# Optimization experiments

Measured on AMD Instinct MI355X. Metric: run time of the kernel, lower is better.

Reference implementation:

```python
import jax, jax.numpy as jnp
import numpy as np

B, P, S, D, L = 8, 64, 512, 512, 64


def setup_inputs() -> dict:
    key = jax.random.key(0)
    ks = jax.random.split(key, 12)
    span_repr = jax.random.normal(ks[0], (B, S, D), dtype=jnp.float32)
    predicates = jax.random.randint(ks[1], (B, P), 0, S, dtype=jnp.int64)
    labels = jax.random.randint(ks[2], (B, P, S), 0, L, dtype=jnp.int64)
    long_mask = jnp.ones((B, P, S), dtype=jnp.int64)
    sc = 1.0 / np.sqrt(D)
    # last-layer weights of FFNN linear_p / linear_a (only last layer matters in source)
    Wp = jax.random.normal(ks[3], (D, D), dtype=jnp.float32) * sc
    bp = jnp.zeros((D,), dtype=jnp.float32)
    Wa = jax.random.normal(ks[4], (D, D), dtype=jnp.float32) * sc
    ba = jnp.zeros((D,), dtype=jnp.float32)
    wp = jax.random.normal(ks[5], (D,), dtype=jnp.float32) * sc  # W_p (Linear D->1, no bias)
    wa = jax.random.normal(ks[6], (D,), dtype=jnp.float32) * sc  # W_a
    W1 = jax.random.normal(ks[7], (L, D, D), dtype=jnp.float32) * sc
    W2 = jax.random.normal(ks[8], (2 * D, L), dtype=jnp.float32) * sc
    b = jax.random.normal(ks[9], (1, L), dtype=jnp.float32) * 0.02
    return {"span_repr": span_repr, "predicates": predicates, "labels": labels,
            "long_mask": long_mask, "Wp": Wp, "bp": bp, "Wa": Wa, "ba": ba,
            "wp": wp, "wa": wa, "W1": W1, "W2": W2, "b": b}


def reference(span_repr, predicates, labels, long_mask, Wp, bp, Wa, ba, wp, wa, W1, W2, b):
    d = span_repr.shape[-1]
    # gather predicate representations: [B, P, D]
    pred_repr = jnp.take_along_axis(span_repr, predicates[..., None], axis=1)
    # FFNN (only last layer is effective in source) + scalar projections
    predicates_score = jax.nn.relu(pred_repr @ Wp.T + bp) @ wp        # [B, P]
    argument_score = jax.nn.relu(span_repr @ Wa.T + ba) @ wa          # [B, S]
    p_a_score = predicates_score[:, :, None] + argument_score[:, None, :]  # [B, P, S]
    # biaffine term: matmul(matmul(pred, W1), span^T) -> [B, P, S, L]
    first = jnp.einsum('bpd,lde,bse->bpsl', pred_repr, W1, span_repr)
    # concat(pred, span) @ W2, split to avoid materializing the concat
    second = (jnp.einsum('bpd,dl->bpl', pred_repr, W2[:d])[:, :, None, :]
              + jnp.einsum('bsd,dl->bsl', span_repr, W2[d:])[:, None, :, :])
    combine = first + second + b + p_a_score[..., None]               # [B, P, S, L]
    combine = combine.at[..., -1].set(0.0)
    num_labels = combine.shape[-1]
    # long_mask is all ones, so masked_select is the full flatten
    stack_instance = combine.reshape(-1, num_labels)                  # [B*P*S, L]
    stack_label = labels.reshape(-1)                                  # [B*P*S]
    return stack_instance, stack_label
```

## Files before the change

### kernel.cpp

```cpp
#include <hip/hip_runtime.h>
#include <hip/hip_bf16.h>

typedef __bf16 bf16x8 __attribute__((ext_vector_type(8)));
typedef float f32x4 __attribute__((ext_vector_type(4)));
typedef unsigned short ushort_t;

#define SS 512
#define DD 512
#define LL 64

__device__ __forceinline__ ushort_t f2b(float f) {
    union { float f; unsigned u; } x; x.f = f;
    unsigned r = x.u + 0x7FFFu + ((x.u >> 16) & 1u);
    return (ushort_t)(r >> 16);
}

__device__ __forceinline__ void async16(const void* g, void* l) {
    __builtin_amdgcn_global_load_lds(
        (const __attribute__((address_space(1))) unsigned int*)g,
        (__attribute__((address_space(3))) unsigned int*)l, 16, 0, 0);
}

__device__ __forceinline__ void stage_tile(const ushort_t* __restrict__ A, int lda,
                                           const ushort_t* __restrict__ Bt, int ldb,
                                           int k0, ushort_t* buf) {
    const int t = threadIdx.x;
    const int wbase = (t >> 6) << 10;
#pragma unroll
    for (int p = 0; p < 2; p++) {
        int row = (p << 7) + (t >> 2);
        int kg = (t & 3) ^ ((t >> 3) & 3);
        async16(A + (size_t)row * lda + k0 + kg * 8,
                (char*)buf + (p << 13) + wbase);
        async16(Bt + (size_t)row * ldb + k0 + kg * 8,
                (char*)(buf + 8192) + (p << 13) + wbase);
    }
}

__device__ __forceinline__ void gemm256(const ushort_t* __restrict__ A, int lda,
                                        const ushort_t* __restrict__ Bt, int ldb,
                                        ushort_t* lds, f32x4 (&acc)[8][4]) {
    const int t = threadIdx.x;
    const int lane = t & 63, wid = t >> 6;
    const int wm = wid >> 2, wn = wid & 3;
    const int r15 = lane & 15, kg = lane >> 4;
    const int sx = ((kg ^ ((r15 >> 1) & 3)) << 4);
    const f32x4 z4 = {0.f, 0.f, 0.f, 0.f};
#pragma unroll
    for (int i = 0; i < 8; i++)
#pragma unroll
        for (int j = 0; j < 4; j++) acc[i][j] = z4;

    stage_tile(A, lda, Bt, ldb, 0, lds);
    stage_tile(A, lda, Bt, ldb, 32, lds + 16384);

    for (int T = 0; T < 16; ++T) {
        if (T < 15) asm volatile("s_waitcnt vmcnt(4)" ::: "memory");
        else        asm volatile("s_waitcnt vmcnt(0)" ::: "memory");
        __builtin_amdgcn_s_barrier();
        __builtin_amdgcn_sched_barrier(0);
        const ushort_t* bufA = lds + (T % 3) * 16384;
        const ushort_t* bufB = bufA + 8192;
        const char* pa = (const char*)bufA + (wm * 128 + r15) * 64 + sx;
        const char* pb = (const char*)bufB + (wn * 64 + r15) * 64 + sx;
        bf16x8 af[8], bf[4];
#pragma unroll
        for (int mf = 0; mf < 8; mf++) af[mf] = *(const bf16x8*)(pa + mf * 1024);
#pragma unroll
        for (int nf = 0; nf < 4; nf++) bf[nf] = *(const bf16x8*)(pb + nf * 1024);
        if (T + 2 < 16)
            stage_tile(A, lda, Bt, ldb, (T + 2) * 32, lds + ((T + 2) % 3) * 16384);
#pragma unroll
        for (int mf = 0; mf < 8; mf++)
#pragma unroll
            for (int nf = 0; nf < 4; nf++)
                acc[mf][nf] = __builtin_amdgcn_mfma_f32_16x16x32_bf16(
                    af[mf], bf[nf], acc[mf][nf], 0, 0, 0);
    }
    __syncthreads();
}

__device__ __forceinline__ void stageA(const ushort_t* __restrict__ A,
                                       int k0, ushort_t* buf) {
    const int t = threadIdx.x;
    const int wbase = (t >> 6) << 10;
#pragma unroll
    for (int p = 0; p < 2; p++) {
        int row = (p << 7) + (t >> 2);
        int kg = (t & 3) ^ ((t >> 3) & 3);
        async16(A + (size_t)row * DD + k0 + kg * 8, (char*)buf + (p << 13) + wbase);
    }
}

__device__ __forceinline__ void gemm256_w1(const ushort_t* __restrict__ predB,
                                           const float* __restrict__ W1le,
                                           ushort_t* lds, f32x4 (&acc)[8][4]) {
    const int t = threadIdx.x;
    const int lane = t & 63, wid = t >> 6;
    const int wm = wid >> 2, wn = wid & 3;
    const int r15 = lane & 15, kg = lane >> 4;
    const int sx = ((kg ^ ((r15 >> 1) & 3)) << 4);
    const f32x4 z4 = {0.f, 0.f, 0.f, 0.f};
#pragma unroll
    for (int i = 0; i < 8; i++)
#pragma unroll
        for (int j = 0; j < 4; j++) acc[i][j] = z4;

    const float* bbase = W1le + (size_t)(kg * 8) * DD + wn * 64 + r15;
    float fb[4][8];
    auto loadB = [&](int k0) {
#pragma unroll
        for (int nf = 0; nf < 4; nf++)
#pragma unroll
            for (int j = 0; j < 8; j++)
                fb[nf][j] = bbase[(size_t)(k0 + j) * DD + nf * 16];
    };

    stageA(predB, 0, lds);
    loadB(0);
    stageA(predB, 32, lds + 8192);

    for (int T = 0; T < 16; ++T) {
        if (T < 15) asm volatile("s_waitcnt vmcnt(2)" ::: "memory");
        else        asm volatile("s_waitcnt vmcnt(0)" ::: "memory");
        __builtin_amdgcn_s_barrier();
        __builtin_amdgcn_sched_barrier(0);
        bf16x8 bf[4];
#pragma unroll
        for (int nf = 0; nf < 4; nf++)
#pragma unroll
            for (int j = 0; j < 8; j++) bf[nf][j] = (__bf16)fb[nf][j];
        if (T + 1 < 16) loadB((T + 1) * 32);
        if (T + 2 < 16) stageA(predB, (T + 2) * 32, lds + ((T + 2) % 3) * 8192);
        const char* pa = (const char*)(lds + (T % 3) * 8192)
                         + (wm * 128 + r15) * 64 + sx;
        bf16x8 af[8];
#pragma unroll
        for (int mf = 0; mf < 8; mf++) af[mf] = *(const bf16x8*)(pa + mf * 1024);
#pragma unroll
        for (int mf = 0; mf < 8; mf++)
#pragma unroll
            for (int nf = 0; nf < 4; nf++)
                acc[mf][nf] = __builtin_amdgcn_mfma_f32_16x16x32_bf16(
                    af[mf], bf[nf], acc[mf][nf], 0, 0, 0);
    }
    __syncthreads();
}

__global__ void __launch_bounds__(512, 2) k_U_small(
    const ushort_t* __restrict__ predB, const float* __restrict__ W1,
    ushort_t* __restrict__ UB,
    const ushort_t* __restrict__ spanB, const ushort_t* __restrict__ WaB,
    const ushort_t* __restrict__ WpB, const ushort_t* __restrict__ W2bT,
    const ushort_t* __restrict__ W2aT,
    const float* __restrict__ ba_, const float* __restrict__ bp_,
    const float* __restrict__ wa, const float* __restrict__ wp,
    float* ascore, float* pscore, float* spanW2, float* predW2) {
    extern __shared__ ushort_t lds[];
    const f32x4 z4 = {0.f, 0.f, 0.f, 0.f};
    const int t = threadIdx.x, lane = t & 63;
    const int r15 = lane & 15, kg = lane >> 4;
    if (blockIdx.x < 256) {
        f32x4 acc[8][4];
        int swz = (blockIdx.x & 7) * 32 + (blockIdx.x >> 3);
        int m0 = (swz & 1) * 256, n0 = (swz >> 1) * 256;
        int l = n0 >> 9, e0 = n0 & 511;
        gemm256_w1(predB + (size_t)m0 * DD, W1 + ((size_t)l * DD) * DD + e0, lds, acc);
        const int wid = t >> 6;
        const int wm = wid >> 2, wn = wid & 3;
        ushort_t* my = lds + wid * 4096;
        int gm = m0 + wm * 128, gn = n0 + wn * 64;
#pragma unroll
        for (int ch = 0; ch < 2; ch++) {
#pragma unroll
            for (int mf2 = 0; mf2 < 4; mf2++)
#pragma unroll
                for (int nf = 0; nf < 4; nf++)
#pragma unroll
                    for (int j = 0; j < 4; j++)
                        my[(mf2 * 16 + kg * 4 + j) * 64 + nf * 16 + r15] =
                            f2b(acc[ch * 4 + mf2][nf][j]);
#pragma unroll
            for (int it = 0; it < 8; it++) {
                int lr = it * 8 + (lane >> 3);
                bf16x8 v = *(const bf16x8*)(my + lr * 64 + (lane & 7) * 8);
                *(bf16x8*)(UB + (size_t)(gm + ch * 64 + lr) * 32768 + gn
                           + (lane & 7) * 8) = v;
            }
        }
        return;
    }
    const bool act = t < 256;
    ushort_t* As = lds;
    ushort_t* Bs = lds + 4096;
    const int wid4 = (t >> 6) & 3;
    const int o0 = wid4 * 1024 + lane * 16;
    int blk = blockIdx.x - 256;
    if (blk < 144) {
        const ushort_t *A, *Bt; const float *bias, *w; float* sc; int m0, n0;
        if (blk < 128) { A = spanB; Bt = WaB; bias = ba_; w = wa; sc = ascore;
                         m0 = (blk >> 2) * 128; n0 = (blk & 3) * 128; }
        else { int q = blk - 128; A = predB; Bt = WpB; bias = bp_; w = wp; sc = pscore;
               m0 = (q >> 2) * 128; n0 = (q & 3) * 128; }
        const ushort_t* Ab = A + (size_t)m0 * DD;
        const ushort_t* Bb = Bt + (size_t)n0 * DD;
        f32x4 acc[4][4];
#pragma unroll
        for (int i = 0; i < 4; i++)
#pragma unroll
            for (int j = 0; j < 4; j++) acc[i][j] = z4;
        int wr = (wid4 >> 1) * 64, wc = (wid4 & 1) * 64;
        for (int k0 = 0; k0 < DD; k0 += 32) {
            if (act) {
#pragma unroll
                for (int p = 0; p < 2; p++) {
                    int o = o0 + p * 4096;
                    async16(Ab + (size_t)(o >> 6) * DD + k0 + ((o & 63) >> 1), (char*)As + o);
                    async16(Bb + (size_t)(o >> 6) * DD + k0 + ((o & 63) >> 1), (char*)Bs + o);
                }
            }
            __syncthreads();
            if (act) {
                bf16x8 af[4], bf[4];
#pragma unroll
                for (int mf = 0; mf < 4; mf++)
                    af[mf] = *(const bf16x8*)(As + (wr + mf * 16 + r15) * 32 + kg * 8);
#pragma unroll
                for (int nf = 0; nf < 4; nf++)
                    bf[nf] = *(const bf16x8*)(Bs + (wc + nf * 16 + r15) * 32 + kg * 8);
#pragma unroll
                for (int mf = 0; mf < 4; mf++)
#pragma unroll
                    for (int nf = 0; nf < 4; nf++)
                        acc[mf][nf] = __builtin_amdgcn_mfma_f32_16x16x32_bf16(
                            af[mf], bf[nf], acc[mf][nf], 0, 0, 0);
            }
            __syncthreads();
        }
        if (act) {
#pragma unroll
            for (int mf = 0; mf < 4; mf++)
#pragma unroll
                for (int j = 0; j < 4; j++) {
                    float v = 0.f;
#pragma unroll
                    for (int nf = 0; nf < 4; nf++) {
                        int col = n0 + wc + nf * 16 + r15;
                        float c = acc[mf][nf][j] + bias[col];
                        if (c > 0.f) v += c * w[col];
                    }
                    v += __shfl_xor(v, 1); v += __shfl_xor(v, 2);
                    v += __shfl_xor(v, 4); v += __shfl_xor(v, 8);
                    if (r15 == 0) atomicAdd(&sc[m0 + wr + mf * 16 + kg * 4 + j], v);
                }
        }
    } else {
        int q = blk - 144;
        const ushort_t *A, *Bt; float* C; int m0;
        if (q < 32) { A = spanB; Bt = W2bT; C = spanW2; m0 = q * 128; }
        else { A = predB; Bt = W2aT; C = predW2; m0 = (q - 32) * 128; }
        const ushort_t* Ab = A + (size_t)m0 * DD;
        f32x4 acc[4][2];
#pragma unroll
        for (int i = 0; i < 4; i++) { acc[i][0] = z4; acc[i][1] = z4; }
        int wr = (wid4 >> 1) * 64, wc = (wid4 & 1) * 32;
        for (int k0 = 0; k0 < DD; k0 += 32) {
            if (act) {
#pragma unroll
                for (int p = 0; p < 2; p++) {
                    int o = o0 + p * 4096;
                    async16(Ab + (size_t)(o >> 6) * DD + k0 + ((o & 63) >> 1), (char*)As + o);
                }
                int o = o0;
                async16(Bt + (size_t)(o >> 6) * DD + k0 + ((o & 63) >> 1), (char*)Bs + o);
            }
            __syncthreads();
            if (act) {
                bf16x8 af[4], bf[2];
#pragma unroll
                for (int mf = 0; mf < 4; mf++)
                    af[mf] = *(const bf16x8*)(As + (wr + mf * 16 + r15) * 32 + kg * 8);
#pragma unroll
                for (int nf = 0; nf < 2; nf++)
                    bf[nf] = *(const bf16x8*)(Bs + (wc + nf * 16 + r15) * 32 + kg * 8);
#pragma unroll
                for (int mf = 0; mf < 4; mf++)
#pragma unroll
                    for (int nf = 0; nf < 2; nf++)
                        acc[mf][nf] = __builtin_amdgcn_mfma_f32_16x16x32_bf16(
                            af[mf], bf[nf], acc[mf][nf], 0, 0, 0);
            }
            __syncthreads();
        }
        if (act) {
#pragma unroll
            for (int mf = 0; mf < 4; mf++)
#pragma unroll
                for (int nf = 0; nf < 2; nf++)
#pragma unroll
                    for (int j = 0; j < 4; j++) {
                        int m = m0 + wr + mf * 16 + kg * 4 + j;
                        int n = wc + nf * 16 + r15;
                        C[(size_t)m * LL + n] = acc[mf][nf][j];
                    }
        }
    }
}

__global__ void __launch_bounds__(512, 2) k_out256(const ushort_t* __restrict__ spanB,
    const ushort_t* __restrict__ UB, const float* __restrict__ spanW2,
    const float* __restrict__ predW2, const float* __restrict__ ascore,
    const float* __restrict__ pscore, const float* __restrict__ bias,
    float* __restrict__ out) {
    extern __shared__ ushort_t lds[];
    f32x4 acc[8][4];
    int swz = (blockIdx.x & 7) * 32 + (blockIdx.x >> 3);
    int b = swz >> 5, r = swz & 31;
    int m0 = (r & 1) * 256, n0 = (r >> 1) * 256;
    gemm256(spanB + ((size_t)b * SS + m0) * DD, DD,
            UB + ((size_t)b * 4096 + n0) * DD, DD, lds, acc);
    const int t = threadIdx.x, lane = t & 63, wid = t >> 6;
    const int wm = wid >> 2, wn = wid & 3, r15 = lane & 15, kg = lane >> 4;
    float cn[4]; int nn[4];
#pragma unroll
    for (int nf = 0; nf < 4; nf++) {
        int n = n0 + wn * 64 + nf * 16 + r15;
        nn[nf] = n;
        cn[nf] = bias[n & 63] + predW2[b * 4096 + n] + pscore[b * 64 + (n >> 6)];
    }
#pragma unroll
    for (int mf = 0; mf < 8; mf++)
#pragma unroll
        for (int j = 0; j < 4; j++) {
            int s = m0 + wm * 128 + mf * 16 + kg * 4 + j;
            float as_ = ascore[b * SS + s];
            const float* sw = spanW2 + ((size_t)b * SS + s) * LL;
#pragma unroll
            for (int nf = 0; nf < 4; nf++) {
                int n = nn[nf], l = n & 63, p = n >> 6;
                float v = acc[mf][nf][j] + cn[nf] + as_ + sw[l];
                if (l == LL - 1) v = 0.f;
                out[(((size_t)b * 64 + p) * SS + s) * LL + l] = v;
            }
        }
}

__global__ __launch_bounds__(256) void k_prep(
    const float* __restrict__ span, const int* __restrict__ preds,
    const int* __restrict__ labels, const float* __restrict__ Wa,
    const float* __restrict__ Wp, const float* __restrict__ W2,
    ushort_t* spanB, ushort_t* predB, ushort_t* WaB, ushort_t* WpB,
    ushort_t* W2aT, ushort_t* W2bT, float* out, float* scores) {
    int blk = blockIdx.x;
    if (blk < 4096) {
        int id = blk * 256 + threadIdx.x;
        if (id < 524288) {
            float4 v = ((const float4*)span)[id];
            ((ushort4*)spanB)[id] = make_ushort4(f2b(v.x), f2b(v.y), f2b(v.z), f2b(v.w));
        } else if (id < 589824) {
            int j = id - 524288;
            int row = j >> 7, c4 = j & 127;
            int b = row >> 6;
            int idx = preds[row];
            float4 v = ((const float4*)(span + ((size_t)(b * SS + idx)) * DD))[c4];
            ((ushort4*)(predB + (size_t)row * DD))[c4] =
                make_ushort4(f2b(v.x), f2b(v.y), f2b(v.z), f2b(v.w));
        } else if (id < 851968) {
            int k = id - 589824;
            out[16777216 + k] = (float)labels[k];
        } else if (id < 917504) {
            int j = id - 851968;
            float4 v = ((const float4*)Wa)[j];
            ((ushort4*)WaB)[j] = make_ushort4(f2b(v.x), f2b(v.y), f2b(v.z), f2b(v.w));
        } else if (id < 983040) {
            int j = id - 917504;
            float4 v = ((const float4*)Wp)[j];
            ((ushort4*)WpB)[j] = make_ushort4(f2b(v.x), f2b(v.y), f2b(v.z), f2b(v.w));
        } else if (id < 1015808) {
            int j = id - 983040;
            W2aT[j] = f2b(W2[(size_t)(j & 511) * LL + (j >> 9)]);
        } else {
            int j = id - 1015808;
            W2bT[j] = f2b(W2[(size_t)((j & 511) + DD) * LL + (j >> 9)]);
        }
    } else {
        int idx = (blk - 4096) * 256 + threadIdx.x;
        if (idx < 4608) scores[idx] = 0.f;
    }
}

extern "C" void kernel_launch(void* const* d_in, const int* in_sizes, int n_in,
                              void* d_out, int out_size, void* d_ws, size_t ws_size,
                              hipStream_t stream) {
    const float* span   = (const float*)d_in[0];
    const int*   preds  = (const int*)d_in[1];
    const int*   labels = (const int*)d_in[2];
    const float* Wp     = (const float*)d_in[4];
    const float* bp_    = (const float*)d_in[5];
    const float* Wa     = (const float*)d_in[6];
    const float* ba_    = (const float*)d_in[7];
    const float* wp     = (const float*)d_in[8];
    const float* wa     = (const float*)d_in[9];
    const float* W1     = (const float*)d_in[10];
    const float* W2     = (const float*)d_in[11];
    const float* bias   = (const float*)d_in[12];
    float* out = (float*)d_out;
    char* ws = (char*)d_ws;

    ushort_t* spanB  = (ushort_t*)(ws + 0);
    ushort_t* predB  = (ushort_t*)(ws + 4194304);
    ushort_t* WaB    = (ushort_t*)(ws + 4718592);
    ushort_t* WpB    = (ushort_t*)(ws + 5242880);
    ushort_t* W2aT   = (ushort_t*)(ws + 5767168);
    ushort_t* W2bT   = (ushort_t*)(ws + 5832704);
    ushort_t* UB     = (ushort_t*)(ws + 39452672);
    float*    ascore = (float*)(ws + 73007104);
    float*    pscore = (float*)(ws + 73023488);
    float*    spanW2 = (float*)(ws + 73025536);
    float*    predW2 = (float*)(ws + 74074112);

    hipFuncSetAttribute((const void*)k_U_small,
                        hipFuncAttributeMaxDynamicSharedMemorySize, 65536);
    hipFuncSetAttribute((const void*)k_out256,
                        hipFuncAttributeMaxDynamicSharedMemorySize, 98304);

    k_prep<<<4114, 256, 0, stream>>>(span, preds, labels, Wa, Wp, W2,
                                     spanB, predB, WaB, WpB, W2aT, W2bT,
                                     out, ascore);

    k_U_small<<<436, 512, 65536, stream>>>(predB, W1, UB,
                                           spanB, WaB, WpB, W2bT, W2aT,
                                           ba_, bp_, wa, wp,
                                           ascore, pscore, spanW2, predW2);

    k_out256<<<256, 512, 98304, stream>>>(spanB, UB, spanW2, predW2,
                                          ascore, pscore, bias, out);
}
```

Measured before the change: 84.25 us.

## Stage W1 tiles through LDS with coalesced float2 loads and double buffering

In the U GEMM, the old code read fp32 W1 straight into registers with strided scalar loads. It now reads W1 with coalesced float2 loads along the row, converts to bf16, and writes a transposed, padded tile (72-byte row pitch) into LDS. The B operand is then read from LDS as MFMA fragments. The A/B pipeline becomes a two-stage double buffer with full vmcnt(0) waits and two barriers per iteration, where before it was a three-stage async pipeline. LDS use grows to 69632 bytes, and the block-to-tile swizzle is changed as well. The aim is to cut uncoalesced global traffic on the large W1 read. The cost is extra LDS writes, more synchronisation, and less prefetch depth.

```diff
diff --git a/kernel.cpp b/kernel.cpp
--- a/kernel.cpp
+++ b/kernel.cpp
@@ -80,8 +80,8 @@
     __syncthreads();
 }
 
-__device__ __forceinline__ void stageA(const ushort_t* __restrict__ A,
-                                       int k0, ushort_t* buf) {
+__device__ __forceinline__ void stageA2(const ushort_t* __restrict__ A,
+                                        int k0, ushort_t* buf) {
     const int t = threadIdx.x;
     const int wbase = (t >> 6) << 10;
 #pragma unroll
@@ -92,9 +92,9 @@
     }
 }
 
-__device__ __forceinline__ void gemm256_w1(const ushort_t* __restrict__ predB,
-                                           const float* __restrict__ W1le,
-                                           ushort_t* lds, f32x4 (&acc)[8][4]) {
+__device__ __forceinline__ void gemm256_w1t(const ushort_t* __restrict__ predB,
+                                            const float* __restrict__ W1g,
+                                            ushort_t* lds, f32x4 (&acc)[8][4]) {
     const int t = threadIdx.x;
     const int lane = t & 63, wid = t >> 6;
     const int wm = wid >> 2, wn = wid & 3;
@@ -106,45 +106,70 @@
 #pragma unroll
         for (int j = 0; j < 4; j++) acc[i][j] = z4;
 
-    const float* bbase = W1le + (size_t)(kg * 8) * DD + wn * 64 + r15;
-    float fb[4][8];
+    const int kpair = t >> 5;
+    const int e2 = (t & 31) * 2;
+    const float* r0base = W1g + (size_t)(2 * kpair) * DD + e2;
+    float2 v0[4], v1[4];
     auto loadB = [&](int k0) {
-#pragma unroll
-        for (int nf = 0; nf < 4; nf++)
-#pragma unroll
-            for (int j = 0; j < 8; j++)
-                fb[nf][j] = bbase[(size_t)(k0 + j) * DD + nf * 16];
+        const float* p0 = r0base + (size_t)k0 * DD;
+        const float* p1 = p0 + DD;
+#pragma unroll
+        for (int i = 0; i < 4; i++) {
+            v0[i] = *(const float2*)(p0 + 64 * i);
+            v1[i] = *(const float2*)(p1 + 64 * i);
+        }
     };
-
-    stageA(predB, 0, lds);
+    auto writeB = [&](ushort_t* bbuf) {
+        char* base = (char*)bbuf;
+#pragma unroll
+        for (int i = 0; i < 4; i++) {
+            int e = e2 + 64 * i;
+            unsigned w0 = (unsigned)f2b(v0[i].x) | ((unsigned)f2b(v1[i].x) << 16);
+            unsigned w1 = (unsigned)f2b(v0[i].y) | ((unsigned)f2b(v1[i].y) << 16);
+            *(unsigned*)(base + (size_t)e * 72 + kpair * 4) = w0;
+            *(unsigned*)(base + (size_t)(e + 1) * 72 + kpair * 4) = w1;
+        }
+    };
+    ushort_t* A0 = lds;            ushort_t* A1 = lds + 8192;
+    ushort_t* B0 = lds + 16384;    ushort_t* B1 = lds + 25600;
+
     loadB(0);
-    stageA(predB, 32, lds + 8192);
+    stageA2(predB, 0, A0);
+    asm volatile("s_waitcnt vmcnt(0)" ::: "memory");
+    writeB(B0);
+    __syncthreads();
 
     for (int T = 0; T < 16; ++T) {
-        if (T < 15) asm volatile("s_waitcnt vmcnt(2)" ::: "memory");
-        else        asm volatile("s_waitcnt vmcnt(0)" ::: "memory");
-        __builtin_amdgcn_s_barrier();
-        __builtin_amdgcn_sched_barrier(0);
+        ushort_t* Acur = (T & 1) ? A1 : A0;
+        ushort_t* Bcur = (T & 1) ? B1 : B0;
+        ushort_t* Anxt = (T & 1) ? A0 : A1;
+        ushort_t* Bnxt = (T & 1) ? B0 : B1;
+        if (T + 1 < 16) { loadB((T + 1) * 32); stageA2(predB, (T + 1) * 32, Anxt); }
+        const char* pa = (const char*)Acur + (wm * 128 + r15) * 64 + sx;
+        bf16x8 af[8];
+#pragma unroll
+        for (int mf = 0; mf < 8; mf++) af[mf] = *(const bf16x8*)(pa + mf * 1024);
         bf16x8 bf[4];
-#pragma unroll
-        for (int nf = 0; nf < 4; nf++)
-#pragma unroll
-            for (int j = 0; j < 8; j++) bf[nf][j] = (__bf16)fb[nf][j];
-        if (T + 1 < 16) loadB((T + 1) * 32);
-        if (T + 2 < 16) stageA(predB, (T + 2) * 32, lds + ((T + 2) % 3) * 8192);
-        const char* pa = (const char*)(lds + (T % 3) * 8192)
-                         + (wm * 128 + r15) * 64 + sx;
-        bf16x8 af[8];
-#pragma unroll
-        for (int mf = 0; mf < 8; mf++) af[mf] = *(const bf16x8*)(pa + mf * 1024);
+        const char* pb = (const char*)Bcur + (size_t)(wn * 64 + r15) * 72 + kg * 16;
+#pragma unroll
+        for (int nf = 0; nf < 4; nf++) {
+            union { bf16x8 v; uint2 q[2]; } u;
+            const char* pn = pb + (size_t)nf * 16 * 72;
+            u.q[0] = *(const uint2*)(pn);
+            u.q[1] = *(const uint2*)(pn + 8);
+            bf[nf] = u.v;
+        }
 #pragma unroll
         for (int mf = 0; mf < 8; mf++)
 #pragma unroll
             for (int nf = 0; nf < 4; nf++)
                 acc[mf][nf] = __builtin_amdgcn_mfma_f32_16x16x32_bf16(
                     af[mf], bf[nf], acc[mf][nf], 0, 0, 0);
-    }
-    __syncthreads();
+        asm volatile("s_waitcnt vmcnt(0)" ::: "memory");
+        __syncthreads();
+        if (T + 1 < 16) writeB(Bnxt);
+        __syncthreads();
+    }
 }
 
 __global__ void __launch_bounds__(512, 2) k_U_small(
@@ -162,10 +187,12 @@
     const int r15 = lane & 15, kg = lane >> 4;
     if (blockIdx.x < 256) {
         f32x4 acc[8][4];
-        int swz = (blockIdx.x & 7) * 32 + (blockIdx.x >> 3);
-        int m0 = (swz & 1) * 256, n0 = (swz >> 1) * 256;
-        int l = n0 >> 9, e0 = n0 & 511;
-        gemm256_w1(predB + (size_t)m0 * DD, W1 + ((size_t)l * DD) * DD + e0, lds, acc);
+        int x = blockIdx.x & 7, s = blockIdx.x >> 3;
+        int m0 = (s & 1) * 256;
+        int nidx = x * 16 + (s >> 1);
+        int n0 = nidx * 256, l = nidx >> 1, e0 = (nidx & 1) * 256;
+        gemm256_w1t(predB + (size_t)m0 * DD,
+                    W1 + (size_t)l * DD * DD + e0, lds, acc);
         const int wid = t >> 6;
         const int wm = wid >> 2, wn = wid & 3;
         ushort_t* my = lds + wid * 4096;
@@ -420,7 +447,7 @@
     float*    predW2 = (float*)(ws + 74074112);
 
     hipFuncSetAttribute((const void*)k_U_small,
-                        hipFuncAttributeMaxDynamicSharedMemorySize, 65536);
+                        hipFuncAttributeMaxDynamicSharedMemorySize, 69632);
     hipFuncSetAttribute((const void*)k_out256,
                         hipFuncAttributeMaxDynamicSharedMemorySize, 98304);
 
@@ -428,7 +455,7 @@
                                      spanB, predB, WaB, WpB, W2aT, W2bT,
                                      out, ascore);
 
-    k_U_small<<<436, 512, 65536, stream>>>(predB, W1, UB,
+    k_U_small<<<436, 512, 69632, stream>>>(predB, W1, UB,
                                            spanB, WaB, WpB, W2bT, W2aT,
                                            ba_, bp_, wa, wp,
                                            ascore, pscore, spanW2, predW2);
```

After: 94.99 us. 1.13x slower.

## Shrink W1 GEMM tiles to 128x128 with 256-thread blocks in k_U_small

Applied to the files above, without the earlier changes.

The U = pred·W1 GEMM in k_U_small moves from 256x256 tiles on 512-thread blocks to 128x128 tiles on 256-thread blocks, giving 1024 tiles instead of 256. The small score and W2 GEMM blocks are now placed first in the grid, and their idle half of threads is removed so every thread participates. The aim is better load balance and occupancy across CUs, with less LDS per block. The cost is that each fp32 W1 element is reloaded by four M-tiles instead of two, and the smaller tiles do fewer MFMAs per byte loaded.

```diff
diff --git a/kernel.cpp b/kernel.cpp
--- a/kernel.cpp
+++ b/kernel.cpp
@@ -80,33 +80,33 @@
     __syncthreads();
 }
 
-__device__ __forceinline__ void stageA(const ushort_t* __restrict__ A,
-                                       int k0, ushort_t* buf) {
+__device__ __forceinline__ void stageA128(const ushort_t* __restrict__ A,
+                                          int k0, ushort_t* buf) {
     const int t = threadIdx.x;
-    const int wbase = (t >> 6) << 10;
 #pragma unroll
     for (int p = 0; p < 2; p++) {
-        int row = (p << 7) + (t >> 2);
+        int row = (p << 6) + (t >> 2);
         int kg = (t & 3) ^ ((t >> 3) & 3);
-        async16(A + (size_t)row * DD + k0 + kg * 8, (char*)buf + (p << 13) + wbase);
-    }
-}
-
-__device__ __forceinline__ void gemm256_w1(const ushort_t* __restrict__ predB,
-                                           const float* __restrict__ W1le,
-                                           ushort_t* lds, f32x4 (&acc)[8][4]) {
+        async16(A + (size_t)row * DD + k0 + kg * 8,
+                (char*)buf + (p << 12) + ((t >> 6) << 10) + (t & 63) * 16);
+    }
+}
+
+__device__ __forceinline__ void gemm128_w1(const ushort_t* __restrict__ predB,
+                                           const float* __restrict__ W1g,
+                                           ushort_t* lds, f32x4 (&acc)[4][4]) {
     const int t = threadIdx.x;
     const int lane = t & 63, wid = t >> 6;
-    const int wm = wid >> 2, wn = wid & 3;
+    const int wm = wid >> 1, wn = wid & 1;
     const int r15 = lane & 15, kg = lane >> 4;
     const int sx = ((kg ^ ((r15 >> 1) & 3)) << 4);
     const f32x4 z4 = {0.f, 0.f, 0.f, 0.f};
 #pragma unroll
-    for (int i = 0; i < 8; i++)
+    for (int i = 0; i < 4; i++)
 #pragma unroll
         for (int j = 0; j < 4; j++) acc[i][j] = z4;
 
-    const float* bbase = W1le + (size_t)(kg * 8) * DD + wn * 64 + r15;
+    const float* bbase = W1g + (size_t)(kg * 8) * DD + wn * 64 + r15;
     float fb[4][8];
     auto loadB = [&](int k0) {
 #pragma unroll
@@ -116,9 +116,9 @@
                 fb[nf][j] = bbase[(size_t)(k0 + j) * DD + nf * 16];
     };
 
-    stageA(predB, 0, lds);
+    stageA128(predB, 0, lds);
     loadB(0);
-    stageA(predB, 32, lds + 8192);
+    stageA128(predB, 32, lds + 4096);
 
     for (int T = 0; T < 16; ++T) {
         if (T < 15) asm volatile("s_waitcnt vmcnt(2)" ::: "memory");
@@ -131,14 +131,14 @@
 #pragma unroll
             for (int j = 0; j < 8; j++) bf[nf][j] = (__bf16)fb[nf][j];
         if (T + 1 < 16) loadB((T + 1) * 32);
-        if (T + 2 < 16) stageA(predB, (T + 2) * 32, lds + ((T + 2) % 3) * 8192);
-        const char* pa = (const char*)(lds + (T % 3) * 8192)
-                         + (wm * 128 + r15) * 64 + sx;
-        bf16x8 af[8];
-#pragma unroll
-        for (int mf = 0; mf < 8; mf++) af[mf] = *(const bf16x8*)(pa + mf * 1024);
-#pragma unroll
-        for (int mf = 0; mf < 8; mf++)
+        if (T + 2 < 16) stageA128(predB, (T + 2) * 32, lds + ((T + 2) % 3) * 4096);
+        const char* pa = (const char*)(lds + (T % 3) * 4096)
+                         + (wm * 64 + r15) * 64 + sx;
+        bf16x8 af[4];
+#pragma unroll
+        for (int mf = 0; mf < 4; mf++) af[mf] = *(const bf16x8*)(pa + mf * 1024);
+#pragma unroll
+        for (int mf = 0; mf < 4; mf++)
 #pragma unroll
             for (int nf = 0; nf < 4; nf++)
                 acc[mf][nf] = __builtin_amdgcn_mfma_f32_16x16x32_bf16(
@@ -147,7 +147,7 @@
     __syncthreads();
 }
 
-__global__ void __launch_bounds__(512, 2) k_U_small(
+__global__ void __launch_bounds__(256) k_U_small(
     const ushort_t* __restrict__ predB, const float* __restrict__ W1,
     ushort_t* __restrict__ UB,
     const ushort_t* __restrict__ spanB, const ushort_t* __restrict__ WaB,
@@ -160,42 +160,41 @@
     const f32x4 z4 = {0.f, 0.f, 0.f, 0.f};
     const int t = threadIdx.x, lane = t & 63;
     const int r15 = lane & 15, kg = lane >> 4;
-    if (blockIdx.x < 256) {
-        f32x4 acc[8][4];
-        int swz = (blockIdx.x & 7) * 32 + (blockIdx.x >> 3);
-        int m0 = (swz & 1) * 256, n0 = (swz >> 1) * 256;
-        int l = n0 >> 9, e0 = n0 & 511;
-        gemm256_w1(predB + (size_t)m0 * DD, W1 + ((size_t)l * DD) * DD + e0, lds, acc);
+    if (blockIdx.x >= 180) {
+        f32x4 acc[4][4];
+        int widx = blockIdx.x - 180;
+        int w = (widx & 7) * 128 + (widx >> 3);
+        int m0 = (w & 3) * 128;
+        int nidx = w >> 2;
+        int n0 = nidx * 128;
+        int l = nidx >> 2, e0 = (nidx & 3) * 128;
+        gemm128_w1(predB + (size_t)m0 * DD,
+                   W1 + (size_t)l * DD * DD + e0, lds, acc);
         const int wid = t >> 6;
-        const int wm = wid >> 2, wn = wid & 3;
+        const int wm = wid >> 1, wn = wid & 1;
         ushort_t* my = lds + wid * 4096;
-        int gm = m0 + wm * 128, gn = n0 + wn * 64;
-#pragma unroll
-        for (int ch = 0; ch < 2; ch++) {
-#pragma unroll
-            for (int mf2 = 0; mf2 < 4; mf2++)
-#pragma unroll
-                for (int nf = 0; nf < 4; nf++)
-#pragma unroll
-                    for (int j = 0; j < 4; j++)
-                        my[(mf2 * 16 + kg * 4 + j) * 64 + nf * 16 + r15] =
-                            f2b(acc[ch * 4 + mf2][nf][j]);
-#pragma unroll
-            for (int it = 0; it < 8; it++) {
-                int lr = it * 8 + (lane >> 3);
-                bf16x8 v = *(const bf16x8*)(my + lr * 64 + (lane & 7) * 8);
-                *(bf16x8*)(UB + (size_t)(gm + ch * 64 + lr) * 32768 + gn
-                           + (lane & 7) * 8) = v;
-            }
+        int gm = m0 + wm * 64, gn = n0 + wn * 64;
+#pragma unroll
+        for (int mf = 0; mf < 4; mf++)
+#pragma unroll
+            for (int nf = 0; nf < 4; nf++)
+#pragma unroll
+                for (int j = 0; j < 4; j++)
+                    my[(mf * 16 + kg * 4 + j) * 64 + nf * 16 + r15] =
+                        f2b(acc[mf][nf][j]);
+#pragma unroll
+        for (int it = 0; it < 8; it++) {
+            int lr = it * 8 + (lane >> 3);
+            bf16x8 v = *(const bf16x8*)(my + lr * 64 + (lane & 7) * 8);
+            *(bf16x8*)(UB + (size_t)(gm + lr) * 32768 + gn + (lane & 7) * 8) = v;
         }
         return;
     }
-    const bool act = t < 256;
     ushort_t* As = lds;
     ushort_t* Bs = lds + 4096;
-    const int wid4 = (t >> 6) & 3;
+    const int wid4 = t >> 6;
     const int o0 = wid4 * 1024 + lane * 16;
-    int blk = blockIdx.x - 256;
+    int blk = blockIdx.x;
     if (blk < 144) {
         const ushort_t *A, *Bt; const float *bias, *w; float* sc; int m0, n0;
         if (blk < 128) { A = spanB; Bt = WaB; bias = ba_; w = wa; sc = ascore;
@@ -211,49 +210,43 @@
             for (int j = 0; j < 4; j++) acc[i][j] = z4;
         int wr = (wid4 >> 1) * 64, wc = (wid4 & 1) * 64;
         for (int k0 = 0; k0 < DD; k0 += 32) {
-            if (act) {
-#pragma unroll
-                for (int p = 0; p < 2; p++) {
-                    int o = o0 + p * 4096;
-                    async16(Ab + (size_t)(o >> 6) * DD + k0 + ((o & 63) >> 1), (char*)As + o);
-                    async16(Bb + (size_t)(o >> 6) * DD + k0 + ((o & 63) >> 1), (char*)Bs + o);
-                }
+#pragma unroll
+            for (int p = 0; p < 2; p++) {
+                int o = o0 + p * 4096;
+                async16(Ab + (size_t)(o >> 6) * DD + k0 + ((o & 63) >> 1), (char*)As + o);
+                async16(Bb + (size_t)(o >> 6) * DD + k0 + ((o & 63) >> 1), (char*)Bs + o);
             }
             __syncthreads();
-            if (act) {
-                bf16x8 af[4], bf[4];
-#pragma unroll
-                for (int mf = 0; mf < 4; mf++)
-                    af[mf] = *(const bf16x8*)(As + (wr + mf * 16 + r15) * 32 + kg * 8);
+            bf16x8 af[4], bf[4];
+#pragma unroll
+            for (int mf = 0; mf < 4; mf++)
+                af[mf] = *(const bf16x8*)(As + (wr + mf * 16 + r15) * 32 + kg * 8);
+#pragma unroll
+            for (int nf = 0; nf < 4; nf++)
+                bf[nf] = *(const bf16x8*)(Bs + (wc + nf * 16 + r15) * 32 + kg * 8);
+#pragma unroll
+            for (int mf = 0; mf < 4; mf++)
 #pragma unroll
                 for (int nf = 0; nf < 4; nf++)
-                    bf[nf] = *(const bf16x8*)(Bs + (wc + nf * 16 + r15) * 32 + kg * 8);
-#pragma unroll
-                for (int mf = 0; mf < 4; mf++)
-#pragma unroll
-                    for (int nf = 0; nf < 4; nf++)
-                        acc[mf][nf] = __builtin_amdgcn_mfma_f32_16x16x32_bf16(
-                            af[mf], bf[nf], acc[mf][nf], 0, 0, 0);
-            }
+                    acc[mf][nf] = __builtin_amdgcn_mfma_f32_16x16x32_bf16(
+                        af[mf], bf[nf], acc[mf][nf], 0, 0, 0);
             __syncthreads();
         }
-        if (act) {
-#pragma unroll
-            for (int mf = 0; mf < 4; mf++)
-#pragma unroll
-                for (int j = 0; j < 4; j++) {
-                    float v = 0.f;
-#pragma unroll
-                    for (int nf = 0; nf < 4; nf++) {
-                        int col = n0 + wc + nf * 16 + r15;
-                        float c = acc[mf][nf][j] + bias[col];
-                        if (c > 0.f) v += c * w[col];
-                    }
-                    v += __shfl_xor(v, 1); v += __shfl_xor(v, 2);
-                    v += __shfl_xor(v, 4); v += __shfl_xor(v, 8);
-                    if (r15 == 0) atomicAdd(&sc[m0 + wr + mf * 16 + kg * 4 + j], v);
+#pragma unroll
+        for (int mf = 0; mf < 4; mf++)
+#pragma unroll
+            for (int j = 0; j < 4; j++) {
+                float v = 0.f;
+#pragma unroll
+                for (int nf = 0; nf < 4; nf++) {
+                    int col = n0 + wc + nf * 16 + r15;
+                    float c = acc[mf][nf][j] + bias[col];
+                    if (c > 0.f) v += c * w[col];
                 }
-        }
+                v += __shfl_xor(v, 1); v += __shfl_xor(v, 2);
+                v += __shfl_xor(v, 4); v += __shfl_xor(v, 8);
+                if (r15 == 0) atomicAdd(&sc[m0 + wr + mf * 16 + kg * 4 + j], v);
+            }
     } else {
         int q = blk - 144;
         const ushort_t *A, *Bt; float* C; int m0;
@@ -265,45 +258,39 @@
         for (int i = 0; i < 4; i++) { acc[i][0] = z4; acc[i][1] = z4; }
         int wr = (wid4 >> 1) * 64, wc = (wid4 & 1) * 32;
         for (int k0 = 0; k0 < DD; k0 += 32) {
-            if (act) {
-#pragma unroll
-                for (int p = 0; p < 2; p++) {
-                    int o = o0 + p * 4096;
-                    async16(Ab + (size_t)(o >> 6) * DD + k0 + ((o & 63) >> 1), (char*)As + o);
-                }
-                int o = o0;
-                async16(Bt + (size_t)(o >> 6) * DD + k0 + ((o & 63) >> 1), (char*)Bs + o);
+#pragma unroll
+            for (int p = 0; p < 2; p++) {
+                int o = o0 + p * 4096;
+                async16(Ab + (size_t)(o >> 6) * DD + k0 + ((o & 63) >> 1), (char*)As + o);
             }
+            int o = o0;
+            async16(Bt + (size_t)(o >> 6) * DD + k0 + ((o & 63) >> 1), (char*)Bs + o);
             __syncthreads();
-            if (act) {
-                bf16x8 af[4], bf[2];
-#pragma unroll
-                for (int mf = 0; mf < 4; mf++)
-                    af[mf] = *(const bf16x8*)(As + (wr + mf * 16 + r15) * 32 + kg * 8);
+            bf16x8 af[4], bf[2];
+#pragma unroll
+            for (int mf = 0; mf < 4; mf++)
+                af[mf] = *(const bf16x8*)(As + (wr + mf * 16 + r15) * 32 + kg * 8);
+#pragma unroll
+            for (int nf = 0; nf < 2; nf++)
+                bf[nf] = *(const bf16x8*)(Bs + (wc + nf * 16 + r15) * 32 + kg * 8);
+#pragma unroll
+            for (int mf = 0; mf < 4; mf++)
 #pragma unroll
                 for (int nf = 0; nf < 2; nf++)
-                    bf[nf] = *(const bf16x8*)(Bs + (wc + nf * 16 + r15) * 32 + kg * 8);
-#pragma unroll
-                for (int mf = 0; mf < 4; mf++)
-#pragma unroll
-                    for (int nf = 0; nf < 2; nf++)
-                        acc[mf][nf] = __builtin_amdgcn_mfma_f32_16x16x32_bf16(
-                            af[mf], bf[nf], acc[mf][nf], 0, 0, 0);
-            }
+                    acc[mf][nf] = __builtin_amdgcn_mfma_f32_16x16x32_bf16(
+                        af[mf], bf[nf], acc[mf][nf], 0, 0, 0);
             __syncthreads();
         }
-        if (act) {
-#pragma unroll
-            for (int mf = 0; mf < 4; mf++)
-#pragma unroll
-                for (int nf = 0; nf < 2; nf++)
-#pragma unroll
-                    for (int j = 0; j < 4; j++) {
-                        int m = m0 + wr + mf * 16 + kg * 4 + j;
-                        int n = wc + nf * 16 + r15;
-                        C[(size_t)m * LL + n] = acc[mf][nf][j];
-                    }
-        }
+#pragma unroll
+        for (int mf = 0; mf < 4; mf++)
+#pragma unroll
+            for (int nf = 0; nf < 2; nf++)
+#pragma unroll
+                for (int j = 0; j < 4; j++) {
+                    int m = m0 + wr + mf * 16 + kg * 4 + j;
+                    int n = wc + nf * 16 + r15;
+                    C[(size_t)m * LL + n] = acc[mf][nf][j];
+                }
     }
 }
 
@@ -420,7 +407,7 @@
     float*    predW2 = (float*)(ws + 74074112);
 
     hipFuncSetAttribute((const void*)k_U_small,
-                        hipFuncAttributeMaxDynamicSharedMemorySize, 65536);
+                        hipFuncAttributeMaxDynamicSharedMemorySize, 32768);
     hipFuncSetAttribute((const void*)k_out256,
                         hipFuncAttributeMaxDynamicSharedMemorySize, 98304);
 
@@ -428,10 +415,10 @@
                                      spanB, predB, WaB, WpB, W2aT, W2bT,
                                      out, ascore);
 
-    k_U_small<<<436, 512, 65536, stream>>>(predB, W1, UB,
-                                           spanB, WaB, WpB, W2bT, W2aT,
-                                           ba_, bp_, wa, wp,
-                                           ascore, pscore, spanW2, predW2);
+    k_U_small<<<1204, 256, 32768, stream>>>(predB, W1, UB,
+                                            spanB, WaB, WpB, W2bT, W2aT,
+                                            ba_, bp_, wa, wp,
+                                            ascore, pscore, spanW2, predW2);
 
     k_out256<<<256, 512, 98304, stream>>>(spanB, UB, spanW2, predW2,
                                           ascore, pscore, bias, out);
```

Measured after the change: 86.88 us. +3.1%, slower.
